# Kernel tuning notes

Hardware: AMD Instinct MI355X
Metric: run time of the kernel (lower is better)

Reference implementation:

```python
import jax, jax.numpy as jnp
import numpy as np

N_NODES = 30522
HID = 768
N_EDGES = 488352
B, S = 4, 512
L = 12  # transformer_layers
C = 100  # num classes in pos-neg codebook graph


def setup_inputs() -> dict:
    key = jax.random.key(0)
    ks = jax.random.split(key, 20)
    inp = {}
    inp["word_embs"] = jax.random.normal(ks[0], (N_NODES, HID), dtype=jnp.float32)
    inp["input_ids"] = jax.random.randint(ks[1], (B, S), 0, N_NODES + 1)  # N_NODES = padding row
    inp["class_ids"] = jax.random.randint(ks[2], (B, S), 0, C + 1)
    inp["mask"] = jax.random.randint(ks[3], (B, S, 1), 0, 2).astype(bool)
    inp["co_edge_index"] = jax.random.randint(ks[4], (2, N_EDGES), 0, N_NODES)
    inp["co_edge_weight"] = jax.random.uniform(ks[5], (N_EDGES,), dtype=jnp.float32)
    inp["re_edge_index"] = jax.random.randint(ks[6], (2, N_EDGES), 0, N_NODES)
    inp["re_edge_weight"] = jax.random.uniform(ks[7], (N_EDGES,), dtype=jnp.float32)
    pn_graph = jax.random.uniform(ks[8], (C + 1, N_NODES), dtype=jnp.float32) * 0.01
    inp["pn_graph"] = pn_graph.at[-1].set(0.0)  # padding row of zeros
    sc = 0.02
    inp["co_W"] = jax.random.normal(ks[9], (3, HID, HID), dtype=jnp.float32) * sc
    inp["co_b"] = jnp.zeros((3, HID), jnp.float32)
    inp["re_W"] = jax.random.normal(ks[10], (3, HID, HID), dtype=jnp.float32) * sc
    inp["re_b"] = jnp.zeros((3, HID), jnp.float32)
    inp["pn_W"] = jax.random.normal(ks[11], (HID, HID), dtype=jnp.float32) * sc  # [out,in] 1x1 conv
    inp["pn_b"] = jnp.zeros((HID,), jnp.float32)
    # zero_convs are zero-initialized in the original; use small random so math is non-trivial
    inp["zero_w"] = jax.random.normal(ks[12], (L, HID, HID), dtype=jnp.float32) * sc
    inp["zero_b"] = jnp.zeros((L, HID), jnp.float32)
    inp["zero_w_pos"] = jax.random.normal(ks[13], (L, HID, HID), dtype=jnp.float32) * sc
    inp["zero_b_pos"] = jnp.zeros((L, HID), jnp.float32)
    return inp


def _gcn_layer(x, src, dst, ew, W, b, n):
    # PyG GCNConv: add self-loops (weight 1), symmetric normalization
    deg = jax.ops.segment_sum(ew, dst, num_segments=n) + 1.0
    dinv = jnp.where(deg > 0, jax.lax.rsqrt(deg), 0.0)
    norm = dinv[src] * ew * dinv[dst]  # [E]
    h = x @ W  # [n, H]
    agg = jax.ops.segment_sum(norm[:, None] * h[src], dst, num_segments=n)
    agg = agg + h * (dinv * dinv)[:, None]  # self-loop contribution
    return agg + b


def _gcn_stack(x, edge_index, ew, Ws, bs, ids):
    src, dst = edge_index[0], edge_index[1]
    n = x.shape[0]
    h = x
    acc = None
    for i in range(3):
        h = jax.nn.relu(_gcn_layer(h, src, dst, ew, Ws[i], bs[i], n))
        pad = jnp.concatenate([h, jnp.zeros((1, h.shape[-1]), h.dtype)], axis=0)
        g = pad[ids]  # [B, S, H] gather with padding row
        acc = g if acc is None else acc + g
    return acc / 3.0


def _zero_conv_layers(tok, w, b):
    # 1x1 conv over hidden channels for each of L layers: [B,S,H] x [L,O,H] -> [L,B,S,O]
    return jnp.einsum("bsh,loh->lbso", tok, w) + b[:, None, None, :]


def reference(word_embs, input_ids, class_ids, mask,
              co_edge_index, co_edge_weight, re_edge_index, re_edge_weight,
              pn_graph, co_W, co_b, re_W, re_b, pn_W, pn_b,
              zero_w, zero_b, zero_w_pos, zero_b_pos):
    Bq, Sq = input_ids.shape
    H = word_embs.shape[-1]
    Lq = zero_w.shape[0]
    inv_mask = (~mask).astype(word_embs.dtype)  # [B,S,1]
    zero_pad = jnp.zeros((Lq, Bq, 1, H), word_embs.dtype)

    co = _gcn_stack(word_embs, co_edge_index, co_edge_weight, co_W, co_b, input_ids)  # [B,S,H]
    re = _gcn_stack(word_embs, re_edge_index, re_edge_weight, re_W, re_b, input_ids)

    # NOTE: original uses self.zero_convs (not a separate set) for BOTH co and re
    co_l = _zero_conv_layers(co, zero_w, zero_b) * inv_mask[None]
    re_l = _zero_conv_layers(re, zero_w, zero_b) * inv_mask[None]
    co_l = jnp.concatenate([zero_pad, co_l], axis=2)  # [L,B,S+1,H]
    re_l = jnp.concatenate([zero_pad, re_l], axis=2)

    # PosNegCodebook: 1x1 conv on codebook, then dense-graph matmul, gathered by class
    cb = word_embs @ pn_W.T + pn_b  # [N, H]
    pn = (pn_graph @ cb)[class_ids]  # [B,S,H] (same math as graph[class_ids] @ cb)
    pn_l = _zero_conv_layers(pn, zero_w_pos, zero_b_pos)
    pn_l = jnp.concatenate([zero_pad, pn_l], axis=2)

    return (co_l, re_l, pn_l)
```

## Files before the change

### kernel.cpp

```cpp
#include <hip/hip_runtime.h>
#include <stdint.h>

typedef unsigned int u32;
typedef unsigned short u16;
typedef __attribute__((ext_vector_type(8))) short short8;
typedef __attribute__((ext_vector_type(4))) float f32x4;

#define N_NODESC 30522
#define HIDC 768
#define NEC 488352
#define TOKM 2048
#define LLAY 12
#define NCLS 101
#define M_PAD 30720
#define ZNC (LLAY*HIDC)
#define OUT_SET (LLAY*4*513*HIDC)
#define PN_KCHUNK 512
#define NBLK 120
#define NN1 (N_NODESC+1)
#define G4_LDS 65536
#define G8_LDS 131072

__device__ __forceinline__ float bl(u32 u){ return __uint_as_float(u<<16); }
__device__ __forceinline__ float bh(u32 u){ return __uint_as_float(u & 0xffff0000u); }
__device__ __forceinline__ u32 f2b1(float f){ u32 x=__float_as_uint(f); return (x + 0x7fffu + ((x>>16)&1u))>>16; }
__device__ __forceinline__ u32 pack2(float a, float b){ return f2b1(a) | (f2b1(b)<<16); }

__device__ __forceinline__ void mfma16(f32x4& d, short8 a, short8 b){
  asm volatile("v_mfma_f32_16x16x32_bf16 %0, %1, %2, %0" : "+v"(d) : "v"(a), "v"(b));
}
__device__ __forceinline__ void async16(const void* g, void* l){
  __builtin_amdgcn_global_load_lds((const __attribute__((address_space(1))) u32*)g,
                                   (__attribute__((address_space(3))) u32*)l, 16, 0, 0);
}
__device__ __forceinline__ void em_dec(double d, int& s, float& w){
  unsigned long long b = __double_as_longlong(d);
  s = (int)(u32)b;
  w = __uint_as_float((u32)(b>>32));
}

__global__ void k_invmask(const void* __restrict__ mask, float* __restrict__ invm){
  __shared__ int s_byte, s_flt;
  int t = threadIdx.x;
  const unsigned char* mb = (const unsigned char*)mask;
  const u32* mw = (const u32*)mask;
  int lb=0, lf=0;
  for(int i=t;i<2048;i+=256) if((i&3)!=0 && mb[i]!=0) lb=1;
  for(int i=t;i<512;i+=256) if(mw[i]==0x3F800000u) lf=1;
  if(t==0){ s_byte=0; s_flt=0; }
  __syncthreads();
  if(lb) s_byte=1;
  if(lf) s_flt=1;
  __syncthreads();
  int mode = s_flt ? 2 : (s_byte ? 1 : 0);
  for(int p=t;p<2048;p+=256){
    int mv = (mode==1) ? (int)mb[p] : (int)(mw[p]!=0u);
    invm[p] = mv ? 0.f : 1.f;
  }
}

__global__ void k_needed(const int* __restrict__ ids, u32* __restrict__ needed,
                         u32* __restrict__ need1,
                         int* __restrict__ tmap, int* __restrict__ nxt){
  int p = blockIdx.x*256 + threadIdx.x;
  if(p < TOKM){
    int id = ids[p];
    if(id < N_NODESC){
      needed[id] = 1u;
      need1[id] = 1u;
      need1[N_NODESC + id] = 1u;
      int old = atomicExch(&tmap[id], p);
      nxt[p] = old;
    }
  }
}

__global__ void k_need_expand(const int* __restrict__ coei, const int* __restrict__ reei,
                              const u32* __restrict__ needed, u32* __restrict__ need1){
  int g = blockIdx.y;
  const int* ei = g ? reei : coei;
  int e = blockIdx.x*256 + threadIdx.x;
  if(e < NEC){
    int d = ei[NEC+e];
    if(needed[d]) need1[(size_t)g*N_NODESC + ei[e]] = 1u;
  }
}

__global__ void k_convAll(const float* __restrict__ pnW, const float* __restrict__ zw,
                          const float* __restrict__ zwp, const float* __restrict__ png,
                          u16* __restrict__ pnwb, u16* __restrict__ zwall,
                          u16* __restrict__ pnb){
  const int NP = HIDC*HIDC/2;
  const int NZ = ZNC*HIDC/2;
  const int NB = 128*(M_PAD/2);
  int i = blockIdx.x*256 + threadIdx.x;
  if(i < NP){
    ((u32*)pnwb)[i] = pack2(pnW[2*i], pnW[2*i+1]);
  } else if(i < NP + NZ){
    int j = i - NP;
    ((u32*)zwall)[j] = pack2(zw[2*j], zw[2*j+1]);
  } else if(i < NP + 2*NZ){
    int j = i - NP - NZ;
    ((u32*)zwall)[NZ + j] = pack2(zwp[2*j], zwp[2*j+1]);
  } else if(i < NP + 2*NZ + NB){
    int j = i - NP - 2*NZ;
    int row = j/(M_PAD/2); int k2 = (j - row*(M_PAD/2))*2;
    float lo=0.f, hi=0.f;
    if(row < NCLS){
      const float* s = png + (size_t)row*N_NODESC;
      if(k2 < N_NODESC) lo = s[k2];
      if(k2+1 < N_NODESC) hi = s[k2+1];
    }
    ((u32*)pnb)[j] = pack2(lo, hi);
  }
}
__global__ void k_conv_pad(const float* __restrict__ src, u16* __restrict__ dst, int srcRows, int padRows){
  int i = blockIdx.x*256 + threadIdx.x;
  if(i >= padRows*384) return;
  int row = i/384; int c2 = (i - row*384)*2;
  float lo=0.f, hi=0.f;
  if(row < srcRows){ const float* s = src + (size_t)row*HIDC + c2; lo=s[0]; hi=s[1]; }
  ((u32*)dst)[i] = pack2(lo, hi);
}
__global__ void k_transposeW2(const float* __restrict__ coW, const float* __restrict__ reW,
                              u16* __restrict__ Wt2){
  int g = blockIdx.y;
  int i = blockIdx.x*256 + threadIdx.x;
  if(i >= 3*HIDC*384) return;
  const float* W = g ? reW : coW;
  int mat = i/(HIDC*384); int rem = i - mat*HIDC*384;
  int n = rem/384; int kd = rem - n*384;
  const float* Wm = W + (size_t)mat*HIDC*HIDC;
  float lo = Wm[(size_t)(2*kd)*HIDC + n];
  float hi = Wm[(size_t)(2*kd+1)*HIDC + n];
  ((u32*)Wt2)[(size_t)g*3*HIDC*384 + (size_t)mat*HIDC*384 + (size_t)n*384 + kd] = pack2(lo, hi);
}

__global__ void k_degcnt2(const int* __restrict__ coei, const int* __restrict__ reei,
                          const float* __restrict__ coew, const float* __restrict__ reew,
                          float* __restrict__ deg2, int* __restrict__ cnt2){
  int g = blockIdx.y;
  const int* ei = g ? reei : coei;
  const float* ew = g ? reew : coew;
  int e = blockIdx.x*256 + threadIdx.x;
  if(e < NEC){ int d = ei[NEC+e]; atomicAdd(&deg2[(size_t)g*N_NODESC + d], ew[e]); atomicAdd(&cnt2[(size_t)g*N_NODESC + d], 1); }
}
__global__ void k_scan1(const int* __restrict__ cnt2, int* __restrict__ part2,
                        const float* __restrict__ deg2,
                        float* __restrict__ dinvA, float* __restrict__ dinvB){
  __shared__ int wt[4];
  int g = blockIdx.y, b = blockIdx.x, t = threadIdx.x;
  int lane = t & 63, w = t >> 6;
  int i = b*256 + t;
  if(i < N_NODESC){
    float d = deg2[(size_t)g*N_NODESC + i] + 1.f;
    dinvA[(size_t)g*N_NODESC + i] = rsqrtf(d);
    dinvB[(size_t)g*N_NODESC + i] = 1.f/d;
  }
  int v = (i < N_NODESC) ? cnt2[(size_t)g*N_NODESC + i] : 0;
  int x = v;
  #pragma unroll
  for(int off=1; off<64; off<<=1){ int y = __shfl_up(x, off); if(lane>=off) x += y; }
  if(lane==63) wt[w] = x;
  __syncthreads();
  if(t==0) part2[g*NBLK + b] = wt[0]+wt[1]+wt[2]+wt[3];
}
__global__ void k_scan2(int* __restrict__ part2, int* __restrict__ rp2){
  __shared__ int w0tot;
  int g = blockIdx.x, t = threadIdx.x;
  int lane = t & 63, w = t >> 6;
  int v = (t < NBLK) ? part2[g*NBLK + t] : 0;
  int x = v;
  #pragma unroll
  for(int off=1; off<64; off<<=1){ int y = __shfl_up(x, off); if(lane>=off) x += y; }
  if(w==0 && lane==63) w0tot = x;
  __syncthreads();
  int incl = x + (w ? w0tot : 0);
  int excl = incl - v;
  if(t < NBLK) part2[g*NBLK + t] = excl;
  if(t == 127) rp2[(size_t)g*NN1 + N_NODESC] = incl;
}
__global__ void k_scan3(const int* __restrict__ cnt2, const int* __restrict__ part2,
                        int* __restrict__ rp2, int* __restrict__ cur2){
  __shared__ int wt[4];
  int g = blockIdx.y, b = blockIdx.x, t = threadIdx.x;
  int lane = t & 63, w = t >> 6;
  int i = b*256 + t;
  int v = (i < N_NODESC) ? cnt2[(size_t)g*N_NODESC + i] : 0;
  int x = v;
  #pragma unroll
  for(int off=1; off<64; off<<=1){ int y = __shfl_up(x, off); if(lane>=off) x += y; }
  if(lane==63) wt[w] = x;
  __syncthreads();
  int wpre = 0;
  #pragma unroll
  for(int j=0;j<4;j++) if(j<w) wpre += wt[j];
  int excl = x - v + wpre + part2[g*NBLK + b];
  if(i < N_NODESC){ rp2[(size_t)g*NN1 + i] = excl; cur2[(size_t)g*N_NODESC + i] = excl; }
}
__global__ void k_scatter2(const int* __restrict__ coei, const int* __restrict__ reei,
                           const float* __restrict__ coew, const float* __restrict__ reew,
                           const float* __restrict__ dinvA, int* __restrict__ cur2,
                           float2* __restrict__ emeta){
  int g = blockIdx.y;
  const int* ei = g ? reei : coei;
  const float* ew = g ? reew : coew;
  int e = blockIdx.x*256 + threadIdx.x;
  if(e < NEC){
    int s = ei[e], d = ei[NEC+e];
    int pos = atomicAdd(&cur2[(size_t)g*N_NODESC + d], 1);
    float nrm = dinvA[(size_t)g*N_NODESC + s]*ew[e]*dinvA[(size_t)g*N_NODESC + d];
    emeta[(size_t)g*NEC + pos] = make_float2(__int_as_float(s), nrm);
  }
}

__global__ __launch_bounds__(256)
void k_spmm2(const u16* __restrict__ hWb, size_t hstride,
             const int* __restrict__ rp2, const float2* __restrict__ emb,
             const float* __restrict__ dinvb,
             const float* __restrict__ bias_co, const float* __restrict__ bias_re,
             u16* __restrict__ houtb, size_t ostride,
             const u32* __restrict__ needarr, const u32* __restrict__ need1,
             const int* __restrict__ tmap, const int* __restrict__ nxt,
             float2* __restrict__ tokfb, size_t tfstride,
             u16* __restrict__ tokall, int phase, int gbase){
  const int g = gbase + blockIdx.y;
  const u16* hW = hWb + (size_t)blockIdx.y*hstride;
  const int* rp = rp2 + (size_t)g*NN1;
  const double* em8 = (const double*)(emb + (size_t)g*NEC);
  const float* dinv2 = dinvb + (size_t)g*N_NODESC;
  const float* bias = (g ? bias_re : bias_co) + phase*HIDC;
  u16* hout = houtb + (size_t)blockIdx.y*ostride;
  const u32* flt = (phase==2) ? needarr : (phase==1 ? need1 + (size_t)g*N_NODESC : nullptr);
  float2* tokf = tokfb + (size_t)blockIdx.y*tfstride;
  u16* tokb = tokall + (size_t)g*TOKM*HIDC;

  int v = blockIdx.x*4 + (threadIdx.x>>6);
  if(v >= N_NODESC) return;
  if(flt && !flt[v]) return;
  int lane = threadIdx.x & 63;
  const u32* H = (const u32*)hW;
  float acc[12];
  #pragma unroll
  for(int q=0;q<12;q++) acc[q]=0.f;
  int e0 = rp[v], e1 = rp[v+1];
  int e = e0;
  for(; e+8<=e1; e+=8){
    int s[8]; float w[8];
    #pragma unroll
    for(int j=0;j<8;j++) em_dec(__builtin_nontemporal_load(em8+e+j), s[j], w[j]);
    const u32* r[8];
    #pragma unroll
    for(int j=0;j<8;j++) r[j] = H + (size_t)s[j]*384 + lane;
    u32 u[8][6];
    #pragma unroll
    for(int j=0;j<8;j++){
      #pragma unroll
      for(int q=0;q<6;q++) u[j][q] = r[j][q*64];
    }
    #pragma unroll
    for(int q=0;q<6;q++){
      acc[2*q]   += w[0]*bl(u[0][q]) + w[1]*bl(u[1][q]) + w[2]*bl(u[2][q]) + w[3]*bl(u[3][q]);
      acc[2*q+1] += w[0]*bh(u[0][q]) + w[1]*bh(u[1][q]) + w[2]*bh(u[2][q]) + w[3]*bh(u[3][q]);
      acc[2*q]   += w[4]*bl(u[4][q]) + w[5]*bl(u[5][q]) + w[6]*bl(u[6][q]) + w[7]*bl(u[7][q]);
      acc[2*q+1] += w[4]*bh(u[4][q]) + w[5]*bh(u[5][q]) + w[6]*bh(u[6][q]) + w[7]*bh(u[7][q]);
    }
  }
  for(; e+4<=e1; e+=4){
    int s0,s1,s2,s3; float w0,w1,w2,w3;
    em_dec(__builtin_nontemporal_load(em8+e  ), s0, w0);
    em_dec(__builtin_nontemporal_load(em8+e+1), s1, w1);
    em_dec(__builtin_nontemporal_load(em8+e+2), s2, w2);
    em_dec(__builtin_nontemporal_load(em8+e+3), s3, w3);
    const u32* r0 = H + (size_t)s0*384 + lane;
    const u32* r1 = H + (size_t)s1*384 + lane;
    const u32* r2 = H + (size_t)s2*384 + lane;
    const u32* r3 = H + (size_t)s3*384 + lane;
    u32 u0[6],u1[6],u2[6],u3[6];
    #pragma unroll
    for(int q=0;q<6;q++){ u0[q]=r0[q*64]; u1[q]=r1[q*64]; u2[q]=r2[q*64]; u3[q]=r3[q*64]; }
    #pragma unroll
    for(int q=0;q<6;q++){
      acc[2*q]   += w0*bl(u0[q]) + w1*bl(u1[q]) + w2*bl(u2[q]) + w3*bl(u3[q]);
      acc[2*q+1] += w0*bh(u0[q]) + w1*bh(u1[q]) + w2*bh(u2[q]) + w3*bh(u3[q]);
    }
  }
  for(; e<e1; ++e){
    int ss; float ww;
    em_dec(__builtin_nontemporal_load(em8+e), ss, ww);
    const u32* r = H + (size_t)ss*384 + lane;
    #pragma unroll
    for(int q=0;q<6;q++){ u32 u = r[q*64]; acc[2*q] += ww*bl(u); acc[2*q+1] += ww*bh(u); }
  }
  { float wgt = dinv2[v];
    const u32* r = H + (size_t)v*384 + lane;
    #pragma unroll
    for(int q=0;q<6;q++){ u32 u = r[q*64]; acc[2*q] += wgt*bl(u); acc[2*q+1] += wgt*bh(u); }
  }
  const float2* B2 = (const float2*)bias;
  u32 wv[6];
  #pragma unroll
  for(int q=0;q<6;q++){
    float2 bb = B2[lane + 64*q];
    float x0 = fmaxf(acc[2*q]+bb.x, 0.f);
    float x1 = fmaxf(acc[2*q+1]+bb.y, 0.f);
    wv[q] = pack2(x0, x1);
  }
  if(phase != 2){
    u32* O = (u32*)hout + (size_t)v*384 + lane;
    #pragma unroll
    for(int q=0;q<6;q++) O[q*64] = wv[q];
  }
  int p = tmap[v];
  while(p >= 0){
    float2* TF = tokf + (size_t)p*384 + lane;
    if(phase == 0){
      #pragma unroll
      for(int q=0;q<6;q++)
        TF[q*64] = make_float2(bl(wv[q])*(1.f/3.f), bh(wv[q])*(1.f/3.f));
    } else if(phase == 1){
      #pragma unroll
      for(int q=0;q<6;q++){
        float2 c = TF[q*64];
        c.x += bl(wv[q])*(1.f/3.f); c.y += bh(wv[q])*(1.f/3.f);
        TF[q*64] = c;
      }
    } else {
      u32* TB = (u32*)tokb + (size_t)p*384 + lane;
      #pragma unroll
      for(int q=0;q<6;q++){
        float2 c = TF[q*64];
        c.x += bl(wv[q])*(1.f/3.f); c.y += bh(wv[q])*(1.f/3.f);
        TB[q*64] = pack2(c.x, c.y);
      }
    }
    p = nxt[p];
  }
}

__global__ void k_gather_pn(const float* __restrict__ GT, const int* __restrict__ cids, u16* __restrict__ tokb){
  int d = blockIdx.x*256 + threadIdx.x;
  if(d >= TOKM*384) return;
  int p = d/384, q = d - p*384;
  int cid = cids[p];
  float lo = GT[(size_t)(2*q)*128 + cid];
  float hi = GT[(size_t)(2*q+1)*128 + cid];
  ((u32*)tokb)[d] = pack2(lo, hi);
}

__device__ __forceinline__ void g_split(int ntM, int ntN, int& bm, int& bn){
  int nwg = ntM*ntN;
  int bid = (int)blockIdx.x;
  int wg = (bid & 7)*(nwg>>3) + (bid>>3);
  if(ntN <= ntM){ bm = wg/ntN; bn = wg - bm*ntN; }
  else          { bn = wg/ntM; bm = wg - bn*ntM; }
}

#define G8_AOFF(b) ((b)*65536)
#define G8_BOFF(b) ((b)*65536 + 32768)

__device__ __forceinline__ void g8_stage(const u16* __restrict__ src, int ldk, int g0, int kt,
                                         char* half_base, int tid){
  const int lane = tid & 63;
  const int csw = ((lane&7) ^ (lane>>3)) << 3;
  const u16* s0 = src + (size_t)(g0 + (tid>>3))*ldk + (kt + csw);
  const u16* s1 = src + (size_t)(g0 + 64 + (tid>>3))*ldk + (kt + csw);
  async16(s0, half_base + (size_t)tid*16);
  async16(s1, half_base + 8192 + (size_t)tid*16);
}

__device__ __forceinline__ void g8_core(const u16* __restrict__ A, const u16* __restrict__ Bt,
                                        int K, int m0, int n0,
                                        f32x4 (&acc)[8][4], char* LDS, int tid){
  const int lane = tid & 63;
  const int wid = tid >> 6;
  const int wr = wid >> 2, wc = wid & 3;
  const int NK = K >> 6;

  g8_stage(Bt, K, n0,      0, LDS + G8_BOFF(0),         tid);
  g8_stage(Bt, K, n0+128,  0, LDS + G8_BOFF(0) + 16384, tid);
  g8_stage(A,  K, m0,      0, LDS + G8_AOFF(0),         tid);
  g8_stage(A,  K, m0+128,  0, LDS + G8_AOFF(0) + 16384, tid);
  g8_stage(Bt, K, n0,     64, LDS + G8_BOFF(1),         tid);
  g8_stage(Bt, K, n0+128, 64, LDS + G8_BOFF(1) + 16384, tid);
  asm volatile("s_waitcnt vmcnt(4)" ::: "memory");
  __builtin_amdgcn_sched_barrier(0);
  __builtin_amdgcn_s_barrier();
  __builtin_amdgcn_sched_barrier(0);

  short8 bf8[8];
  for(int T=0; T<NK; ++T){
    const int buf = T & 1;
    const char* Ab = LDS + G8_AOFF(buf) + wr*16384;
    const char* Bb = LDS + G8_BOFF(buf) + (wc>>1)*16384;
    #pragma unroll
    for(int q=0; q<4; ++q){
      if(q==0){
        #pragma unroll
        for(int n=0;n<4;n++){
          #pragma unroll
          for(int kk=0;kk<2;kk++){
            int row = ((wc&1)<<6) + (n<<4) + (lane&15);
            int cb = ((kk<<6) + ((lane>>4)<<4)) ^ ((lane&7)<<4);
            bf8[n*2+kk] = *(const short8*)(Bb + row*128 + cb);
          }
        }
      }
      short8 af[2][2];
      #pragma unroll
      for(int j=0;j<2;j++){
        #pragma unroll
        for(int kk=0;kk<2;kk++){
          int row = ((2*q+j)<<4) + (lane&15);
          int cb = ((kk<<6) + ((lane>>4)<<4)) ^ ((lane&7)<<4);
          af[j][kk] = *(const short8*)(Ab + row*128 + cb);
        }
      }
      if(q==0 && T+1<NK) g8_stage(A,  K, m0,      (T+1)<<6, LDS + G8_AOFF((T+1)&1),         tid);
      if(q==1 && T+1<NK) g8_stage(A,  K, m0+128,  (T+1)<<6, LDS + G8_AOFF((T+1)&1) + 16384, tid);
      if(q==2 && T+2<NK) g8_stage(Bt, K, n0,      (T+2)<<6, LDS + G8_BOFF(buf),             tid);
      if(q==3 && T+2<NK) g8_stage(Bt, K, n0+128,  (T+2)<<6, LDS + G8_BOFF(buf) + 16384,     tid);
      if(q==3){
        if(T <= NK-3)      asm volatile("s_waitcnt vmcnt(4)" ::: "memory");
        else if(T == NK-2) asm volatile("s_waitcnt vmcnt(0)" ::: "memory");
      }
      __builtin_amdgcn_sched_barrier(0);
      __builtin_amdgcn_s_barrier();
      __builtin_amdgcn_sched_barrier(0);
      __builtin_amdgcn_s_setprio(1);
      #pragma unroll
      for(int j=0;j<2;j++){
        #pragma unroll
        for(int n=0;n<4;n++){
          #pragma unroll
          for(int kk=0;kk<2;kk++) mfma16(acc[2*q+j][n], af[j][kk], bf8[n*2+kk]);
        }
      }
      __builtin_amdgcn_s_setprio(0);
      __builtin_amdgcn_sched_barrier(0);
      __builtin_amdgcn_s_barrier();
      __builtin_amdgcn_sched_barrier(0);
    }
  }
}

__global__ __launch_bounds__(512,2)
void gemm8p_zc(const u16* __restrict__ TOKALL, const u16* __restrict__ ZWALL,
               const float* __restrict__ zb, const float* __restrict__ zbp,
               const float* __restrict__ invm, float* __restrict__ out){
  extern __shared__ char LDS[];
  const int set = blockIdx.z;
  const u16* A  = TOKALL + (size_t)set*TOKM*HIDC;
  const u16* Bt = ZWALL + (set==2 ? (size_t)ZNC*HIDC : 0);
  const float* bias = (set==2) ? zbp : zb;
  const bool use_mask = (set != 2);
  float* o = out + (size_t)set*OUT_SET;

  const int tid = threadIdx.x;
  const int lane = tid & 63;
  const int wid = tid >> 6;
  const int wr = wid >> 2, wc = wid & 3;
  int bm, bn;
  g_split(TOKM>>8, ZNC>>8, bm, bn);
  const int m0 = bm << 8, n0 = bn << 8;

  f32x4 acc[8][4];
  f32x4 zv = {0.f,0.f,0.f,0.f};
  #pragma unroll
  for(int m=0;m<8;m++){
    #pragma unroll
    for(int n=0;n<4;n++) acc[m][n] = zv;
  }
  g8_core(A, Bt, HIDC, m0, n0, acc, LDS, tid);

  const int l = n0 / HIDC;
  const int oc0 = n0 - l*HIDC;
  const int lo = lane & 15, hi = lane >> 4;

  #pragma unroll
  for(int pass=0; pass<2; ++pass){
    __syncthreads();
    if(wr == pass){
      #pragma unroll
      for(int m=0;m<8;m++){
        #pragma unroll
        for(int n=0;n<4;n++){
          int col = (wc<<6) + (n<<4) + lo;
          float badd = bias[n0 + col];
          #pragma unroll
          for(int r=0;r<4;r++){
            int lr = (m<<4) + (hi<<2) + r;
            *(float*)(LDS + (size_t)lr*1024 + ((col<<2) ^ ((lr&7)<<4))) = acc[m][n][r] + badd;
          }
        }
      }
    }
    __syncthreads();
    #pragma unroll
    for(int i=0;i<16;i++){
      int lr = (i<<3) + wid;
      int rr = m0 + (pass<<7) + lr;
      int b = rr >> 9, s = rr & 511;
      f32x4 v = *(const f32x4*)(LDS + (size_t)lr*1024 + ((lane<<4) ^ ((lr&7)<<4)));
      if(use_mask){ float w = invm[rr]; v = v * w; }
      *(f32x4*)(o + (size_t)((l*4+b)*513 + (s+1))*HIDC + oc0 + (lane<<2)) = v;
      if(s == 0){
        f32x4 z4 = {0.f,0.f,0.f,0.f};
        *(f32x4*)(o + (size_t)((l*4+b)*513)*HIDC + oc0 + (lane<<2)) = z4;
      }
    }
  }
}

#define G4_ABUF(b) ((b)*32768)
#define G4_BBUF(b) ((b)*32768 + 16384)

__device__ __forceinline__ void g4_stage(const u16* __restrict__ src, int ldk, int g0, int kt,
                                         char* base, int tid){
  const int lane = tid & 63;
  const int csw = ((lane&7) ^ (lane>>3)) << 3;
  const int r = tid >> 3;
  #pragma unroll
  for(int h=0; h<4; ++h)
    async16(src + (size_t)(g0 + h*32 + r)*ldk + (kt + csw), base + h*4096 + (size_t)tid*16);
}

__device__ __forceinline__ void g4_core(const u16* __restrict__ A, const u16* __restrict__ Bt,
                                        int K, int m0, int n0,
                                        f32x4 (&acc)[4][4], char* LDS, int tid){
  const int lane = tid & 63;
  const int wid = tid >> 6;
  const int wr = wid >> 1, wc = wid & 1;
  const int NK = K >> 6;

  g4_stage(A,  K, m0,  0, LDS + G4_ABUF(0), tid);
  g4_stage(Bt, K, n0,  0, LDS + G4_BBUF(0), tid);
  g4_stage(A,  K, m0, 64, LDS + G4_ABUF(1), tid);
  g4_stage(Bt, K, n0, 64, LDS + G4_BBUF(1), tid);

  short8 af[4][2], bf[4][2];
  for(int T=0; T<NK; ++T){
    const int buf = T & 1;
    const char* Ab = LDS + G4_ABUF(buf) + wr*8192;
    const char* Bb = LDS + G4_BBUF(buf) + wc*8192;
    if(T+1 < NK) asm volatile("s_waitcnt vmcnt(8)" ::: "memory");
    else         asm volatile("s_waitcnt vmcnt(0)" ::: "memory");
    __builtin_amdgcn_sched_barrier(0);
    __builtin_amdgcn_s_barrier();
    __builtin_amdgcn_sched_barrier(0);
    #pragma unroll
    for(int m=0;m<4;m++){
      #pragma unroll
      for(int kk=0;kk<2;kk++){
        int row = (m<<4) + (lane&15);
        int cb = ((kk<<6) + ((lane>>4)<<4)) ^ ((lane&7)<<4);
        af[m][kk] = *(const short8*)(Ab + row*128 + cb);
        bf[m][kk] = *(const short8*)(Bb + row*128 + cb);
      }
    }
    asm volatile("s_waitcnt lgkmcnt(0)" ::: "memory");
    __builtin_amdgcn_sched_barrier(0);
    __builtin_amdgcn_s_setprio(1);
    #pragma unroll
    for(int m=0;m<2;m++){
      #pragma unroll
      for(int n=0;n<4;n++){
        #pragma unroll
        for(int kk=0;kk<2;kk++) mfma16(acc[m][n], af[m][kk], bf[n][kk]);
      }
    }
    __builtin_amdgcn_s_setprio(0);
    __builtin_amdgcn_sched_barrier(0);
    __builtin_amdgcn_s_barrier();
    __builtin_amdgcn_sched_barrier(0);
    if(T+2 < NK){
      g4_stage(A,  K, m0, (T+2)<<6, LDS + G4_ABUF(buf), tid);
      g4_stage(Bt, K, n0, (T+2)<<6, LDS + G4_BBUF(buf), tid);
    }
    __builtin_amdgcn_s_setprio(1);
    #pragma unroll
    for(int m=2;m<4;m++){
      #pragma unroll
      for(int n=0;n<4;n++){
        #pragma unroll
        for(int kk=0;kk<2;kk++) mfma16(acc[m][n], af[m][kk], bf[n][kk]);
      }
    }
    __builtin_amdgcn_s_setprio(0);
    __builtin_amdgcn_sched_barrier(0);
  }
}

__global__ __launch_bounds__(256,2)
void gemm4p_bias(const u16* __restrict__ A, const u16* __restrict__ Bt,
                 int M, int N, int K,
                 u16* __restrict__ outB, const float* __restrict__ bias){
  extern __shared__ char LDS[];
  const int tid = threadIdx.x;
  const int lane = tid & 63;
  const int wid = tid >> 6;
  const int wr = wid >> 1, wc = wid & 1;
  int bm, bn;
  g_split(M>>7, N>>7, bm, bn);
  const int m0 = bm << 7, n0 = bn << 7;

  f32x4 acc[4][4];
  f32x4 zv = {0.f,0.f,0.f,0.f};
  #pragma unroll
  for(int m=0;m<4;m++){
    #pragma unroll
    for(int n=0;n<4;n++) acc[m][n] = zv;
  }
  g4_core(A, Bt, K, m0, n0, acc, LDS, tid);

  const int rbase = (lane>>4)<<2;
  const int cbase = lane & 15;
  #pragma unroll
  for(int m=0;m<4;m++){
    int row0 = m0 + (wr<<6) + (m<<4) + rbase;
    #pragma unroll
    for(int n=0;n<4;n++){
      int col = n0 + (wc<<6) + (n<<4) + cbase;
      #pragma unroll
      for(int r=0;r<4;r++){
        float v = acc[m][n][r] + bias[row0+r];
        outB[(size_t)(row0+r)*N + col] = (u16)f2b1(v);
      }
    }
  }
}

__global__ __launch_bounds__(256,2)
void gemm4p_gcn(const u16* __restrict__ Xb, size_t xstride,
                const u16* __restrict__ wt2, int layer,
                u16* __restrict__ outb, size_t ostride, int gbase){
  extern __shared__ char LDS[];
  const int g = gbase + blockIdx.z;
  const u16* A = Xb + (size_t)blockIdx.z*xstride;
  const u16* Bt = wt2 + ((size_t)g*3 + layer)*HIDC*HIDC;
  u16* outB = outb + (size_t)blockIdx.z*ostride;

  const int tid = threadIdx.x;
  const int lane = tid & 63;
  const int wid = tid >> 6;
  const int wr = wid >> 1, wc = wid & 1;
  int bm, bn;
  g_split(M_PAD>>7, HIDC>>7, bm, bn);
  const int m0 = bm << 7, n0 = bn << 7;

  f32x4 acc[4][4];
  f32x4 zv = {0.f,0.f,0.f,0.f};
  #pragma unroll
  for(int m=0;m<4;m++){
    #pragma unroll
    for(int n=0;n<4;n++) acc[m][n] = zv;
  }
  g4_core(A, Bt, HIDC, m0, n0, acc, LDS, tid);

  const int rbase = (lane>>4)<<2;
  const int cbase = lane & 15;
  #pragma unroll
  for(int m=0;m<4;m++){
    int row0 = m0 + (wr<<6) + (m<<4) + rbase;
    #pragma unroll
    for(int n=0;n<4;n++){
      int col = n0 + (wc<<6) + (n<<4) + cbase;
      #pragma unroll
      for(int r=0;r<4;r++)
        outB[(size_t)(row0+r)*HIDC + col] = (u16)f2b1(acc[m][n][r]);
    }
  }
}

__global__ __launch_bounds__(256,2)
void gemm_splitk(const u16* __restrict__ A, const u16* __restrict__ Bt,
                 int M, int N, int K, float* __restrict__ outF, int kchunk){
  __shared__ u16 As[128*64];
  __shared__ u16 Bs[128*64];
  const int t = threadIdx.x;
  const int lane = t & 63;
  const int w = t >> 6;
  const int wr = w >> 1, wc = w & 1;
  int nchunks = (K + kchunk - 1)/kchunk;
  int bm = (int)blockIdx.x / nchunks;
  int ch = (int)blockIdx.x - bm*nchunks;
  int k0 = ch*kchunk, k1 = k0 + kchunk; if(k1 > K) k1 = K;
  const int m0 = bm << 7, n0 = 0;

  f32x4 zv = {0.f,0.f,0.f,0.f};
  f32x4 acc[4][4];
  #pragma unroll
  for(int m=0;m<4;m++){
    #pragma unroll
    for(int n=0;n<4;n++) acc[m][n] = zv;
  }
  const int srow = t >> 3;
  const int scol = (t & 7) << 3;
  const u16* Ag = A + (size_t)(m0 + srow)*K + scol;
  const u16* Bg = Bt + (size_t)(n0 + srow)*K + scol;
  u16* Al = &As[t*8];
  u16* Bl = &Bs[t*8];

  for(int kt=k0; kt<k1; kt+=64){
    __syncthreads();
    #pragma unroll
    for(int i=0;i<4;i++){
      async16(Ag + (size_t)(i*32)*K + kt, Al + i*2048);
      async16(Bg + (size_t)(i*32)*K + kt, Bl + i*2048);
    }
    __syncthreads();
    #pragma unroll
    for(int kk=0; kk<64; kk+=32){
      const int ko = kk + ((lane>>4)<<3);
      short8 af[4], bfv[4];
      #pragma unroll
      for(int m=0;m<4;m++) af[m] = *(const short8*)&As[((wr<<6)+(m<<4)+(lane&15))*64 + ko];
      #pragma unroll
      for(int n=0;n<4;n++) bfv[n] = *(const short8*)&Bs[((wc<<6)+(n<<4)+(lane&15))*64 + ko];
      #pragma unroll
      for(int m=0;m<4;m++){
        #pragma unroll
        for(int n=0;n<4;n++) mfma16(acc[m][n], af[m], bfv[n]);
      }
    }
  }
  const int rbase = (lane>>4)<<2;
  const int cbase = lane & 15;
  #pragma unroll
  for(int m=0;m<4;m++){
    int row0 = m0 + (wr<<6) + (m<<4) + rbase;
    #pragma unroll
    for(int n=0;n<4;n++){
      int col = n0 + (wc<<6) + (n<<4) + cbase;
      #pragma unroll
      for(int r=0;r<4;r++) atomicAdd(&outF[(size_t)(row0+r)*N + col], acc[m][n][r]);
    }
  }
}

extern "C" void kernel_launch(void* const* d_in, const int* in_sizes, int n_in,
                              void* d_out, int out_size, void* d_ws, size_t ws_size,
                              hipStream_t stream){
  const float* word  = (const float*)d_in[0];
  const int*   ids   = (const int*)d_in[1];
  const int*   cids  = (const int*)d_in[2];
  const void*  mask  = d_in[3];
  const int*   co_ei = (const int*)d_in[4];
  const float* co_ew = (const float*)d_in[5];
  const int*   re_ei = (const int*)d_in[6];
  const float* re_ew = (const float*)d_in[7];
  const float* png   = (const float*)d_in[8];
  const float* co_W  = (const float*)d_in[9];
  const float* co_b  = (const float*)d_in[10];
  const float* re_W  = (const float*)d_in[11];
  const float* re_b  = (const float*)d_in[12];
  const float* pn_W  = (const float*)d_in[13];
  const float* pn_b  = (const float*)d_in[14];
  const float* zw    = (const float*)d_in[15];
  const float* zb    = (const float*)d_in[16];
  const float* zwp   = (const float*)d_in[17];
  const float* zbp   = (const float*)d_in[18];
  float* out = (float*)d_out;

  hipFuncSetAttribute((const void*)gemm4p_bias, hipFuncAttributeMaxDynamicSharedMemorySize, G4_LDS);
  hipFuncSetAttribute((const void*)gemm4p_gcn,  hipFuncAttributeMaxDynamicSharedMemorySize, G4_LDS);
  hipFuncSetAttribute((const void*)gemm8p_zc,   hipFuncAttributeMaxDynamicSharedMemorySize, G8_LDS);

  const size_t MH = (size_t)M_PAD*HIDC;
  const size_t TFS = (size_t)TOKM*384;
  const bool batched = ws_size >= ((size_t)340 << 20);

  char* wsb = (char*)d_ws;
  size_t off = 0;
  auto alloc = [&](size_t bytes)->void*{ void* p = wsb + off; off += (bytes + 255) & ~(size_t)255; return p; };
  u16* WORDB = (u16*)alloc(MH*2);
  u16* BUFB  = (u16*)alloc(MH*2*(batched?2:1));
  u16* BUFX  = (u16*)alloc(MH*2*(batched?2:1));
  u16* ZWALL = (u16*)alloc((size_t)2*ZNC*HIDC*2);
  u16* WT2   = (u16*)alloc((size_t)2*3*HIDC*HIDC*2);
  u16* PNWB  = (u16*)alloc((size_t)HIDC*HIDC*2);
  u16* PNB   = (u16*)alloc((size_t)128*M_PAD*2);
  u16* TOKALL= (u16*)alloc((size_t)3*TOKM*HIDC*2);
  float2* TOKF = (float2*)alloc(TFS*8*(batched?2:1));
  size_t zg0 = off;
  u32*   NEED = (u32*)alloc((size_t)N_NODESC*4);
  u32*   NEED1= (u32*)alloc((size_t)2*N_NODESC*4);
  float* DEG2 = (float*)alloc((size_t)2*N_NODESC*4);
  int*   CNT2 = (int*)alloc((size_t)2*N_NODESC*4);
  float* GT   = (float*)alloc((size_t)HIDC*128*4);
  size_t zg_bytes = off - zg0;
  float* DINVA = (float*)alloc((size_t)2*N_NODESC*4);
  float* DINVB = (float*)alloc((size_t)2*N_NODESC*4);
  int*   RP2  = (int*)alloc((size_t)2*NN1*4);
  int*   CUR2 = (int*)alloc((size_t)2*N_NODESC*4);
  int*   PART2= (int*)alloc((size_t)2*NBLK*4);
  float2* EMETA=(float2*)alloc((size_t)2*NEC*8);
  int*   TMAP = (int*)alloc((size_t)N_NODESC*4);
  int*   NXT  = (int*)alloc((size_t)TOKM*4);
  float* INVM = (float*)alloc((size_t)TOKM*4);
  (void)ws_size; (void)in_sizes; (void)n_in; (void)out_size;

  const int GD_TOK = (TOKM*384 + 255)/256;
  const int GD_E   = (NEC + 255)/256;
  const int SPMM_GD  = (N_NODESC + 3)/4;
  const int PN_NCHUNKS = M_PAD/PN_KCHUNK;
  const int G_PN  = (HIDC/128)*PN_NCHUNKS;
  const int G4_GCN = (M_PAD/128)*(HIDC/128);
  const int G4_CBT = (HIDC/128)*(M_PAD/128);
  const int G8_ZC  = (TOKM/256)*(ZNC/256);
  const int NCONVALL = HIDC*HIDC/2 + 2*(ZNC*HIDC/2) + 128*(M_PAD/2);

  hipMemsetAsync(wsb + zg0, 0, zg_bytes, stream);
  hipMemsetAsync(TMAP, 0xFF, (size_t)N_NODESC*4, stream);
  hipMemsetAsync(TOKALL, 0, (size_t)2*TOKM*HIDC*2, stream);
  k_invmask<<<1,256,0,stream>>>(mask, INVM);
  k_needed<<<(TOKM+255)/256,256,0,stream>>>(ids, NEED, NEED1, TMAP, NXT);
  k_need_expand<<<dim3(GD_E,2),256,0,stream>>>(co_ei, re_ei, NEED, NEED1);
  k_convAll<<<(NCONVALL + 255)/256,256,0,stream>>>(pn_W, zw, zwp, png, PNWB, ZWALL, PNB);
  k_conv_pad<<<(M_PAD*384 + 255)/256,256,0,stream>>>(word, WORDB, N_NODESC, M_PAD);
  k_transposeW2<<<dim3((3*HIDC*384 + 255)/256, 2),256,0,stream>>>(co_W, re_W, WT2);

  k_degcnt2<<<dim3(GD_E,2),256,0,stream>>>(co_ei, re_ei, co_ew, re_ew, DEG2, CNT2);
  k_scan1<<<dim3(NBLK,2),256,0,stream>>>(CNT2, PART2, DEG2, DINVA, DINVB);
  k_scan2<<<2,128,0,stream>>>(PART2, RP2);
  k_scan3<<<dim3(NBLK,2),256,0,stream>>>(CNT2, PART2, RP2, CUR2);
  k_scatter2<<<dim3(GD_E,2),256,0,stream>>>(co_ei, re_ei, co_ew, re_ew, DINVA, CUR2, EMETA);

  gemm4p_bias<<<G4_CBT,256,G4_LDS,stream>>>(PNWB, WORDB, HIDC, M_PAD, HIDC, BUFX, pn_b);
  gemm_splitk<<<G_PN,256,0,stream>>>(BUFX, PNB, HIDC, 128, M_PAD, GT, PN_KCHUNK);
  k_gather_pn<<<GD_TOK,256,0,stream>>>(GT, cids, TOKALL + (size_t)2*TOKM*HIDC);

  if(batched){
    for(int i=0;i<3;i++){
      gemm4p_gcn<<<dim3(G4_GCN,1,2),256,G4_LDS,stream>>>(
          (i==0)? WORDB : BUFX, (i==0)? 0 : MH, WT2, i, BUFB, MH, 0);
      k_spmm2<<<dim3(SPMM_GD,2),256,0,stream>>>(
          BUFB, MH, RP2, EMETA, DINVB, co_b, re_b, BUFX, MH,
          NEED, NEED1, TMAP, NXT, TOKF, TFS, TOKALL, i, 0);
    }
  } else {
    for(int g=0; g<2; ++g){
      const u16* X = WORDB;
      for(int i=0;i<3;i++){
        gemm4p_gcn<<<dim3(G4_GCN,1,1),256,G4_LDS,stream>>>(X, 0, WT2, i, BUFB, 0, g);
        k_spmm2<<<dim3(SPMM_GD,1),256,0,stream>>>(
            BUFB, 0, RP2, EMETA, DINVB, co_b, re_b, BUFX, 0,
            NEED, NEED1, TMAP, NXT, TOKF, 0, TOKALL, i, g);
        X = BUFX;
      }
    }
  }

  dim3 zgrid(G8_ZC, 1, 3);
  gemm8p_zc<<<zgrid,512,G8_LDS,stream>>>(TOKALL, ZWALL, zb, zbp, INVM, out);
}
```

Measured before the change: 1.088 ms.

## Replace pipelined 256x256 zero-conv GEMM with simpler 128x256 single-buffer kernel

The zero-conv GEMM moves from a 256x256 tile with a double-buffered, carefully interleaved async-load pipeline and 128KB of LDS to a 128x256 tile. The new kernel uses single-buffered 48KB staging with plain syncthreads and launch bounds that allow 4 blocks. The goal is higher occupancy and twice as many workgroups, letting several resident blocks hide memory latency instead of explicit software pipelining. In exchange, loads no longer overlap compute within a block, and each block reuses data less, which raises global traffic for the weight matrix.

```diff
diff --git a/kernel.cpp b/kernel.cpp
--- a/kernel.cpp
+++ b/kernel.cpp
@@ -19,7 +19,7 @@
 #define NBLK 120
 #define NN1 (N_NODESC+1)
 #define G4_LDS 65536
-#define G8_LDS 131072
+#define ZC_LDS 65536
 
 __device__ __forceinline__ float bl(u32 u){ return __uint_as_float(u<<16); }
 __device__ __forceinline__ float bh(u32 u){ return __uint_as_float(u & 0xffff0000u); }
@@ -356,98 +356,21 @@
   else          { bn = wg/ntM; bm = wg - bn*ntM; }
 }
 
-#define G8_AOFF(b) ((b)*65536)
-#define G8_BOFF(b) ((b)*65536 + 32768)
-
-__device__ __forceinline__ void g8_stage(const u16* __restrict__ src, int ldk, int g0, int kt,
-                                         char* half_base, int tid){
-  const int lane = tid & 63;
-  const int csw = ((lane&7) ^ (lane>>3)) << 3;
-  const u16* s0 = src + (size_t)(g0 + (tid>>3))*ldk + (kt + csw);
-  const u16* s1 = src + (size_t)(g0 + 64 + (tid>>3))*ldk + (kt + csw);
-  async16(s0, half_base + (size_t)tid*16);
-  async16(s1, half_base + 8192 + (size_t)tid*16);
-}
-
-__device__ __forceinline__ void g8_core(const u16* __restrict__ A, const u16* __restrict__ Bt,
-                                        int K, int m0, int n0,
-                                        f32x4 (&acc)[8][4], char* LDS, int tid){
-  const int lane = tid & 63;
-  const int wid = tid >> 6;
-  const int wr = wid >> 2, wc = wid & 3;
-  const int NK = K >> 6;
-
-  g8_stage(Bt, K, n0,      0, LDS + G8_BOFF(0),         tid);
-  g8_stage(Bt, K, n0+128,  0, LDS + G8_BOFF(0) + 16384, tid);
-  g8_stage(A,  K, m0,      0, LDS + G8_AOFF(0),         tid);
-  g8_stage(A,  K, m0+128,  0, LDS + G8_AOFF(0) + 16384, tid);
-  g8_stage(Bt, K, n0,     64, LDS + G8_BOFF(1),         tid);
-  g8_stage(Bt, K, n0+128, 64, LDS + G8_BOFF(1) + 16384, tid);
-  asm volatile("s_waitcnt vmcnt(4)" ::: "memory");
-  __builtin_amdgcn_sched_barrier(0);
-  __builtin_amdgcn_s_barrier();
-  __builtin_amdgcn_sched_barrier(0);
-
-  short8 bf8[8];
-  for(int T=0; T<NK; ++T){
-    const int buf = T & 1;
-    const char* Ab = LDS + G8_AOFF(buf) + wr*16384;
-    const char* Bb = LDS + G8_BOFF(buf) + (wc>>1)*16384;
-    #pragma unroll
-    for(int q=0; q<4; ++q){
-      if(q==0){
-        #pragma unroll
-        for(int n=0;n<4;n++){
-          #pragma unroll
-          for(int kk=0;kk<2;kk++){
-            int row = ((wc&1)<<6) + (n<<4) + (lane&15);
-            int cb = ((kk<<6) + ((lane>>4)<<4)) ^ ((lane&7)<<4);
-            bf8[n*2+kk] = *(const short8*)(Bb + row*128 + cb);
-          }
-        }
-      }
-      short8 af[2][2];
-      #pragma unroll
-      for(int j=0;j<2;j++){
-        #pragma unroll
-        for(int kk=0;kk<2;kk++){
-          int row = ((2*q+j)<<4) + (lane&15);
-          int cb = ((kk<<6) + ((lane>>4)<<4)) ^ ((lane&7)<<4);
-          af[j][kk] = *(const short8*)(Ab + row*128 + cb);
-        }
-      }
-      if(q==0 && T+1<NK) g8_stage(A,  K, m0,      (T+1)<<6, LDS + G8_AOFF((T+1)&1),         tid);
-      if(q==1 && T+1<NK) g8_stage(A,  K, m0+128,  (T+1)<<6, LDS + G8_AOFF((T+1)&1) + 16384, tid);
-      if(q==2 && T+2<NK) g8_stage(Bt, K, n0,      (T+2)<<6, LDS + G8_BOFF(buf),             tid);
-      if(q==3 && T+2<NK) g8_stage(Bt, K, n0+128,  (T+2)<<6, LDS + G8_BOFF(buf) + 16384,     tid);
-      if(q==3){
-        if(T <= NK-3)      asm volatile("s_waitcnt vmcnt(4)" ::: "memory");
-        else if(T == NK-2) asm volatile("s_waitcnt vmcnt(0)" ::: "memory");
-      }
-      __builtin_amdgcn_sched_barrier(0);
-      __builtin_amdgcn_s_barrier();
-      __builtin_amdgcn_sched_barrier(0);
-      __builtin_amdgcn_s_setprio(1);
-      #pragma unroll
-      for(int j=0;j<2;j++){
-        #pragma unroll
-        for(int n=0;n<4;n++){
-          #pragma unroll
-          for(int kk=0;kk<2;kk++) mfma16(acc[2*q+j][n], af[j][kk], bf8[n*2+kk]);
-        }
-      }
-      __builtin_amdgcn_s_setprio(0);
-      __builtin_amdgcn_sched_barrier(0);
-      __builtin_amdgcn_s_barrier();
-      __builtin_amdgcn_sched_barrier(0);
-    }
-  }
-}
-
-__global__ __launch_bounds__(512,2)
-void gemm8p_zc(const u16* __restrict__ TOKALL, const u16* __restrict__ ZWALL,
-               const float* __restrict__ zb, const float* __restrict__ zbp,
-               const float* __restrict__ invm, float* __restrict__ out){
+template<int NCH>
+__device__ __forceinline__ void z_stage(const u16* __restrict__ src, int ldk, int g0, int kt,
+                                        char* base, int tid){
+  const int c = tid & 7;
+  const int r = (tid >> 3) & 63;
+  const int csw = (c ^ (r & 7)) << 3;
+  #pragma unroll
+  for(int h=0; h<NCH; ++h)
+    async16(src + (size_t)(g0 + h*64 + r)*ldk + (kt + csw), base + h*8192 + (size_t)tid*16);
+}
+
+__global__ __launch_bounds__(512,4)
+void gemm_zc2(const u16* __restrict__ TOKALL, const u16* __restrict__ ZWALL,
+              const float* __restrict__ zb, const float* __restrict__ zbp,
+              const float* __restrict__ invm, float* __restrict__ out){
   extern __shared__ char LDS[];
   const int set = blockIdx.z;
   const u16* A  = TOKALL + (size_t)set*TOKM*HIDC;
@@ -461,17 +384,54 @@
   const int wid = tid >> 6;
   const int wr = wid >> 2, wc = wid & 3;
   int bm, bn;
-  g_split(TOKM>>8, ZNC>>8, bm, bn);
-  const int m0 = bm << 8, n0 = bn << 8;
-
-  f32x4 acc[8][4];
+  g_split(TOKM>>7, ZNC>>8, bm, bn);
+  const int m0 = bm << 7, n0 = bn << 8;
+
+  char* LA = LDS;
+  char* LB = LDS + 16384;
+
+  f32x4 acc[4][4];
   f32x4 zv = {0.f,0.f,0.f,0.f};
   #pragma unroll
-  for(int m=0;m<8;m++){
+  for(int m=0;m<4;m++){
     #pragma unroll
     for(int n=0;n<4;n++) acc[m][n] = zv;
   }
-  g8_core(A, Bt, HIDC, m0, n0, acc, LDS, tid);
+
+  const int NK = HIDC >> 6;
+  for(int T=0; T<NK; ++T){
+    __syncthreads();
+    z_stage<2>(A,  HIDC, m0, T<<6, LA, tid);
+    z_stage<4>(Bt, HIDC, n0, T<<6, LB, tid);
+    __syncthreads();
+    const char* Ab = LA + (wr<<13);
+    const char* Bb = LB + (wc<<13);
+    short8 bf[4][2];
+    #pragma unroll
+    for(int n=0;n<4;n++){
+      #pragma unroll
+      for(int kk=0;kk<2;kk++){
+        int row = (n<<4) + (lane&15);
+        int cb = ((kk<<6) + ((lane>>4)<<4)) ^ ((lane&7)<<4);
+        bf[n][kk] = *(const short8*)(Bb + row*128 + cb);
+      }
+    }
+    #pragma unroll
+    for(int m=0;m<4;m++){
+      short8 af[2];
+      #pragma unroll
+      for(int kk=0;kk<2;kk++){
+        int row = (m<<4) + (lane&15);
+        int cb = ((kk<<6) + ((lane>>4)<<4)) ^ ((lane&7)<<4);
+        af[kk] = *(const short8*)(Ab + row*128 + cb);
+      }
+      #pragma unroll
+      for(int n=0;n<4;n++){
+        #pragma unroll
+        for(int kk=0;kk<2;kk++) mfma16(acc[m][n], af[kk], bf[n][kk]);
+      }
+    }
+  }
 
   const int l = n0 / HIDC;
   const int oc0 = n0 - l*HIDC;
@@ -482,7 +442,7 @@
     __syncthreads();
     if(wr == pass){
       #pragma unroll
-      for(int m=0;m<8;m++){
+      for(int m=0;m<4;m++){
         #pragma unroll
         for(int n=0;n<4;n++){
           int col = (wc<<6) + (n<<4) + lo;
@@ -497,9 +457,9 @@
     }
     __syncthreads();
     #pragma unroll
-    for(int i=0;i<16;i++){
+    for(int i=0;i<8;i++){
       int lr = (i<<3) + wid;
-      int rr = m0 + (pass<<7) + lr;
+      int rr = m0 + (pass<<6) + lr;
       int b = rr >> 9, s = rr & 511;
       f32x4 v = *(const f32x4*)(LDS + (size_t)lr*1024 + ((lane<<4) ^ ((lr&7)<<4)));
       if(use_mask){ float w = invm[rr]; v = v * w; }
@@ -764,7 +724,7 @@
 
   hipFuncSetAttribute((const void*)gemm4p_bias, hipFuncAttributeMaxDynamicSharedMemorySize, G4_LDS);
   hipFuncSetAttribute((const void*)gemm4p_gcn,  hipFuncAttributeMaxDynamicSharedMemorySize, G4_LDS);
-  hipFuncSetAttribute((const void*)gemm8p_zc,   hipFuncAttributeMaxDynamicSharedMemorySize, G8_LDS);
+  hipFuncSetAttribute((const void*)gemm_zc2,    hipFuncAttributeMaxDynamicSharedMemorySize, ZC_LDS);
 
   const size_t MH = (size_t)M_PAD*HIDC;
   const size_t TFS = (size_t)TOKM*384;
@@ -807,7 +767,7 @@
   const int G_PN  = (HIDC/128)*PN_NCHUNKS;
   const int G4_GCN = (M_PAD/128)*(HIDC/128);
   const int G4_CBT = (HIDC/128)*(M_PAD/128);
-  const int G8_ZC  = (TOKM/256)*(ZNC/256);
+  const int G_ZC2  = (TOKM/128)*(ZNC/256);
   const int NCONVALL = HIDC*HIDC/2 + 2*(ZNC*HIDC/2) + 128*(M_PAD/2);
 
   hipMemsetAsync(wsb + zg0, 0, zg_bytes, stream);
@@ -851,6 +811,6 @@
     }
   }
 
-  dim3 zgrid(G8_ZC, 1, 3);
-  gemm8p_zc<<<zgrid,512,G8_LDS,stream>>>(TOKALL, ZWALL, zb, zbp, INVM, out);
-}
+  dim3 zgrid(G_ZC2, 1, 3);
+  gemm_zc2<<<zgrid,512,ZC_LDS,stream>>>(TOKALL, ZWALL, zb, zbp, INVM, out);
+}
```

Result: no change. 1.090 ms (+0.1%).
